# Performance work log

Measured on AMD Instinct MI355X. Metric: run time of the kernel, lower is better.

The kernel has to match this reference:

```python
import jax, jax.numpy as jnp
import numpy as np

BH, W, C, NHEAD = 512, 256, 128, 4
HEAD_DIM = C // NHEAD
EPS = 1e-5


def _xavier(key, shape):
    fan_out, fan_in = shape
    lim = np.sqrt(6.0 / (fan_in + fan_out)).astype(np.float32)
    return jax.random.uniform(key, shape, jnp.float32, -lim, lim)


def setup_inputs() -> dict:
    key = jax.random.key(0)
    ks = jax.random.split(key, 4)
    return {
        "feat_left": jax.random.normal(ks[0], (BH, W, C), jnp.float32),
        "feat_right": jax.random.normal(ks[1], (BH, W, C), jnp.float32),
        "l_proj_weight": _xavier(ks[2], (2 * C, C)),
        "r_proj_weight": _xavier(ks[3], (2 * C, C)),
        "l_proj_bias": jnp.zeros((2 * C,), jnp.float32),
        "r_proj_bias": jnp.zeros((2 * C,), jnp.float32),
        "l_out_weight": _xavier(jax.random.fold_in(key, 10), (C, C)),
        "l_out_bias": jnp.zeros((C,), jnp.float32),
        "r_out_weight": _xavier(jax.random.fold_in(key, 11), (C, C)),
        "r_out_bias": jnp.zeros((C,), jnp.float32),
        "norm_weight": jnp.ones((C,), jnp.float32),
        "norm_bias": jnp.zeros((C,), jnp.float32),
    }


def _layernorm(x, w, b):
    mu = jnp.mean(x, axis=-1, keepdims=True)
    var = jnp.mean(jnp.square(x - mu), axis=-1, keepdims=True)
    return (x - mu) * jax.lax.rsqrt(var + EPS) * w + b


def reference(feat_left, feat_right, l_proj_weight, r_proj_weight,
              l_proj_bias, r_proj_bias, l_out_weight, l_out_bias,
              r_out_weight, r_out_bias, norm_weight, norm_bias):
    bh, w, c = feat_left.shape
    e, hd = NHEAD, HEAD_DIM

    l_n = _layernorm(feat_left, norm_weight, norm_bias)
    r_n = _layernorm(feat_right, norm_weight, norm_bias)

    l_kv = l_n @ l_proj_weight.T + l_proj_bias
    r_kv = r_n @ r_proj_weight.T + r_proj_bias
    l_k, l_v = jnp.split(l_kv, 2, axis=-1)
    r_k, r_v = jnp.split(r_kv, 2, axis=-1)

    l_k = l_k.reshape(bh, w, e, hd)
    r_k = r_k.reshape(bh, w, e, hd)
    l_v = l_v.reshape(bh, w, e, hd)
    r_v = r_v.reshape(bh, w, e, hd)

    # shared score matrix [bh, heads, w_left, w_right]
    attn = jnp.einsum('nwec,nvec->newv', l_k, r_k) * 0.1

    # left attends over right positions (softmax over last axis)
    sm_l = jax.nn.softmax(attn, axis=-1)
    out_l = jnp.einsum('newv,nvec->nwec', sm_l, r_v).reshape(bh, w, c)

    # right attends over left positions (softmax over w axis of same scores)
    sm_r = jax.nn.softmax(attn, axis=2)
    out_r = jnp.einsum('newv,nwec->nvec', sm_r, l_v).reshape(bh, w, c)

    out_l = out_l @ l_out_weight.T + l_out_bias
    out_r = out_r @ r_out_weight.T + r_out_bias

    return feat_left + out_l, feat_right + out_r
```

## Files before the change

### kernel.cpp

```cpp
#include <hip/hip_runtime.h>
#include <hip/hip_bf16.h>

#define BH   512
#define NW   256
#define CC   128
#define TOK  (BH * NW)

typedef __attribute__((ext_vector_type(8))) short short8;
typedef __attribute__((ext_vector_type(4))) float f32x4;
typedef __attribute__((ext_vector_type(4))) int   i32x4;
typedef __attribute__((ext_vector_type(4))) unsigned short us4;
typedef __attribute__((ext_vector_type(2))) unsigned int u32x2;
typedef unsigned short ushort_t;

static __device__ __forceinline__ f32x4 mfma16(short8 a, short8 b, f32x4 c) {
    return __builtin_amdgcn_mfma_f32_16x16x32_bf16(a, b, c, 0, 0, 0);
}

static __device__ __forceinline__ unsigned int pk2(float a, float b) {
    __hip_bfloat162 h = __float22bfloat162_rn(make_float2(a, b));
    return *reinterpret_cast<unsigned int*>(&h);
}
static __device__ __forceinline__ ushort_t f2bf(float f) {
    unsigned int u = __float_as_uint(f);
    u = (u + 0x7fffu + ((u >> 16) & 1u)) >> 16;
    return (ushort_t)u;
}
#if __has_builtin(__builtin_amdgcn_exp2f)
static __device__ __forceinline__ float exp2_fast(float x) { return __builtin_amdgcn_exp2f(x); }
#else
static __device__ __forceinline__ float exp2_fast(float x) { return exp2f(x); }
#endif

__global__ __launch_bounds__(256)
void k_prep(const float* __restrict__ WpL, const float* __restrict__ WpR,
            const float* __restrict__ bpL, const float* __restrict__ bpR,
            const float* __restrict__ nw,  const float* __restrict__ nb,
            ushort_t* __restrict__ Wb, float* __restrict__ bias2)
{
    const int gid = blockIdx.x * 256 + threadIdx.x;
    const int row = gid >> 2;
    const int q   = gid & 3;
    const int side = row >> 8;
    const int o    = row & 255;
    const float* Wp = side ? WpR : WpL;
    const float* bp = side ? bpR : bpL;
    const float* wr = Wp + (size_t)o * 128 + q * 32;

    float acc = 0.f;
#pragma unroll
    for (int g = 0; g < 4; ++g) {
        const int c = q * 32 + g * 8;
        float4 wa = *(const float4*)(wr + g * 8);
        float4 wb = *(const float4*)(wr + g * 8 + 4);
        float4 ga = *(const float4*)(nw + c);
        float4 gb = *(const float4*)(nw + c + 4);
        float4 ba = *(const float4*)(nb + c);
        float4 bb = *(const float4*)(nb + c + 4);
        acc += wa.x*ba.x + wa.y*ba.y + wa.z*ba.z + wa.w*ba.w
             + wb.x*bb.x + wb.y*bb.y + wb.z*bb.z + wb.w*bb.w;
        u32x2 o0, o1;
        o0[0] = pk2(wa.x*ga.x, wa.y*ga.y);
        o0[1] = pk2(wa.z*ga.z, wa.w*ga.w);
        o1[0] = pk2(wb.x*gb.x, wb.y*gb.y);
        o1[1] = pk2(wb.z*gb.z, wb.w*gb.w);
        *(u32x2*)(Wb + (size_t)row * 128 + c)     = o0;
        *(u32x2*)(Wb + (size_t)row * 128 + c + 4) = o1;
    }
    acc += __shfl_xor(acc, 1);
    acc += __shfl_xor(acc, 2);
    if (q == 0) bias2[row] = bp[o] + acc;
}

__global__ __launch_bounds__(512)
void k_ln_proj(const float* __restrict__ featL, const float* __restrict__ featR,
               const ushort_t* __restrict__ Wb, const float* __restrict__ bias2,
               ushort_t* __restrict__ kvL,      ushort_t* __restrict__ kvR)
{
    const int side = blockIdx.y;
    const float* feat = side ? featR : featL;
    const ushort_t* W = Wb + side * 32768;
    const float* b2   = bias2 + side * 256;
    ushort_t*    kv   = side ? kvR : kvL;

    const int m0  = blockIdx.x * 64;
    const int tid = threadIdx.x;
    const int wid = tid >> 6, lane = tid & 63, l16 = lane & 15, lh = lane >> 4;
    const int wn  = wid * 32;

    __shared__ ushort_t Asm[64][136];

    const int row = tid >> 3, q = tid & 7;
    const float* fr = feat + (size_t)(m0 + row) * CC + q * 16;
    float x[16];
#pragma unroll
    for (int i = 0; i < 4; ++i) {
        float4 v = *(const float4*)(fr + i * 4);
        x[i*4+0]=v.x; x[i*4+1]=v.y; x[i*4+2]=v.z; x[i*4+3]=v.w;
    }

    short8 Bf[8];
#pragma unroll
    for (int kk = 0; kk < 4; ++kk)
#pragma unroll
        for (int tn = 0; tn < 2; ++tn)
            Bf[kk*2 + tn] = *(const short8*)(W + (size_t)(wn + tn*16 + l16) * CC + kk*32 + lh*8);
    float4 bias[2];
#pragma unroll
    for (int tn = 0; tn < 2; ++tn)
        bias[tn] = *(const float4*)(b2 + wn + tn*16 + lh*4);

    {
        float s = 0.f, s2 = 0.f;
#pragma unroll
        for (int i = 0; i < 16; ++i) { s += x[i]; s2 += x[i]*x[i]; }
#pragma unroll
        for (int m = 1; m < 8; m <<= 1) { s += __shfl_xor(s, m); s2 += __shfl_xor(s2, m); }
        float mu   = s * (1.f / 128.f);
        float var  = s2 * (1.f / 128.f) - mu * mu;
        float rstd = rsqrtf(var + 1e-5f);
        float a = rstd, bsh = -mu * rstd;
#pragma unroll
        for (int g = 0; g < 2; ++g) {
            i32x4 o;
#pragma unroll
            for (int k = 0; k < 4; ++k)
                o[k] = (int)pk2(x[g*8 + 2*k] * a + bsh, x[g*8 + 2*k + 1] * a + bsh);
            *(i32x4*)&Asm[row][q * 16 + g * 8] = o;
        }
    }
    __syncthreads();

    f32x4 acc[4][2];
#pragma unroll
    for (int mt = 0; mt < 4; ++mt)
#pragma unroll
        for (int tn = 0; tn < 2; ++tn)
            acc[mt][tn] = (f32x4){0.f, 0.f, 0.f, 0.f};

#pragma unroll
    for (int kk = 0; kk < 4; ++kk) {
        short8 a[4];
#pragma unroll
        for (int mt = 0; mt < 4; ++mt)
            a[mt] = *(const short8*)&Asm[mt*16 + l16][kk*32 + lh*8];
#pragma unroll
        for (int tn = 0; tn < 2; ++tn)
#pragma unroll
            for (int mt = 0; mt < 4; ++mt)
                acc[mt][tn] = mfma16(Bf[kk*2 + tn], a[mt], acc[mt][tn]);
    }

    const float kscale = (side == 0 && wn < 128) ? 0.14426950408889634f : 1.0f;
#pragma unroll
    for (int mt = 0; mt < 4; ++mt) {
        const int token = m0 + mt*16 + l16;
#pragma unroll
        for (int tn = 0; tn < 2; ++tn) {
            const int f0 = wn + tn*16 + lh*4;
            float v0 = (acc[mt][tn][0] + bias[tn].x) * kscale;
            float v1 = (acc[mt][tn][1] + bias[tn].y) * kscale;
            float v2 = (acc[mt][tn][2] + bias[tn].z) * kscale;
            float v3 = (acc[mt][tn][3] + bias[tn].w) * kscale;
            u32x2 wv;
            wv[0] = pk2(v0, v1);
            wv[1] = pk2(v2, v3);
            *(u32x2*)(kv + (size_t)token * 256 + f0) = wv;
        }
    }
}

template<int BF16OUT>
__global__ __launch_bounds__(512, 4)
void k_attn(const ushort_t* __restrict__ kvL, const ushort_t* __restrict__ kvR,
            float* __restrict__ outFBase, ushort_t* __restrict__ outBBase)
{
    const int bx   = blockIdx.x;
    const int work = (bx & 7) * 512 + (bx >> 3);
    const int n    = work >> 3;
    const int e    = (work >> 1) & 3;
    const int dir  = work & 1;
    const ushort_t* kvA = dir ? kvR : kvL;
    const ushort_t* kvB = dir ? kvL : kvR;

    const int tid = threadIdx.x;
    const int wid = tid >> 6, lane = tid & 63, l16 = lane & 15, lh = lane >> 4;
    const int W0 = wid * 32;
    const int kcls = (l16 >> 1) & 3;

    __shared__ ushort_t kB[256][32];
    __shared__ ushort_t vT[32][280];
    __shared__ ushort_t pL[8][32][32];

    {
        const ushort_t* src = kvB + (size_t)n * 256 * 256 + e * 32;
#pragma unroll
        for (int p = 0; p < 2; ++p) {
            int u = tid + p * 512;
            int r = u >> 2, slot = u & 3;
            *(i32x4*)&kB[r][(slot ^ ((r >> 1) & 3)) << 3] =
                *(const i32x4*)(src + (size_t)r * 256 + slot * 8);
        }
    }
    {
        const ushort_t* src = kvB + (size_t)n * 256 * 256 + 128 + e * 32;
#pragma unroll
        for (int u4 = 0; u4 < 4; ++u4) {
            int unit = tid + u4 * 512;
            int cp = unit & 15, vp = unit >> 4;
            unsigned int w0 = *(const unsigned int*)(src + (size_t)(vp*2    ) * 256 + cp*2);
            unsigned int w1 = *(const unsigned int*)(src + (size_t)(vp*2 + 1) * 256 + cp*2);
            *(unsigned int*)&vT[cp*2    ][vp*2] = (w0 & 0xffffu) | (w1 << 16);
            *(unsigned int*)&vT[cp*2 + 1][vp*2] = (w0 >> 16) | (w1 & 0xffff0000u);
        }
    }
    short8 aK[2];
#pragma unroll
    for (int tr = 0; tr < 2; ++tr)
        aK[tr] = *(const short8*)(kvA + (size_t)(n*256 + W0 + tr*16 + l16) * 256 + e*32 + lh*8);

    short8 ones;
#pragma unroll
    for (int i = 0; i < 8; ++i) ones[i] = (short)0x3F80;

    __syncthreads();

    f32x4 oacc[2][2];
#pragma unroll
    for (int tr = 0; tr < 2; ++tr)
#pragma unroll
        for (int ct = 0; ct < 2; ++ct)
            oacc[tr][ct] = (f32x4){0.f, 0.f, 0.f, 0.f};
    f32x4 lacc[2] = {(f32x4){0.f,0.f,0.f,0.f}, (f32x4){0.f,0.f,0.f,0.f}};

#pragma unroll 2
    for (int nc = 0; nc < 8; ++nc) {
        const int vc0 = nc * 32;

        short8 bk0 = *(const short8*)&kB[vc0      + l16][(lh ^ kcls) << 3];
        short8 bk1 = *(const short8*)&kB[vc0 + 16 + l16][(lh ^ kcls) << 3];
        f32x4 s[2][2];
#pragma unroll
        for (int tr = 0; tr < 2; ++tr) {
            s[tr][0] = mfma16(bk0, aK[tr], (f32x4){0.f,0.f,0.f,0.f});
            s[tr][1] = mfma16(bk1, aK[tr], (f32x4){0.f,0.f,0.f,0.f});
        }

#pragma unroll
        for (int tr = 0; tr < 2; ++tr) {
            const int prow = tr*16 + l16;
#pragma unroll
            for (int tc = 0; tc < 2; ++tc) {
                float p0 = exp2_fast(s[tr][tc][0]);
                float p1 = exp2_fast(s[tr][tc][1]);
                float p2 = exp2_fast(s[tr][tc][2]);
                float p3 = exp2_fast(s[tr][tc][3]);
                u32x2 w;
                w[0] = pk2(p0, p1);
                w[1] = pk2(p2, p3);
                const int sL   = 2*tc + (lh >> 1);
                const int pcol = ((sL ^ kcls) << 3) + ((lh & 1) << 2);
                *(u32x2*)&pL[wid][prow][pcol] = w;
            }
        }

        short8 aP[2], bV[2];
#pragma unroll
        for (int tr = 0; tr < 2; ++tr)
            aP[tr] = *(const short8*)&pL[wid][tr*16 + l16][(lh ^ kcls) << 3];
#pragma unroll
        for (int ct = 0; ct < 2; ++ct)
            bV[ct] = *(const short8*)&vT[ct*16 + l16][vc0 + lh*8];
#pragma unroll
        for (int tr = 0; tr < 2; ++tr) {
#pragma unroll
            for (int ct = 0; ct < 2; ++ct)
                oacc[tr][ct] = mfma16(bV[ct], aP[tr], oacc[tr][ct]);
            lacc[tr] = mfma16(ones, aP[tr], lacc[tr]);
        }
    }

#pragma unroll
    for (int tr = 0; tr < 2; ++tr) {
        float rinv = 1.f / lacc[tr][0];
        const int token = n * 256 + W0 + tr*16 + l16;
        if (BF16OUT) {
            ushort_t* outB = outBBase + (size_t)dir * TOK * CC;
#pragma unroll
            for (int ct = 0; ct < 2; ++ct) {
                us4 o;
#pragma unroll
                for (int j = 0; j < 4; ++j)
                    o[j] = f2bf(oacc[tr][ct][j] * rinv);
                *(us4*)(outB + (size_t)token * CC + e*32 + ct*16 + lh*4) = o;
            }
        } else {
            float* outF = outFBase + (size_t)dir * TOK * CC;
#pragma unroll
            for (int ct = 0; ct < 2; ++ct) {
                float4 o;
                o.x = oacc[tr][ct][0] * rinv;
                o.y = oacc[tr][ct][1] * rinv;
                o.z = oacc[tr][ct][2] * rinv;
                o.w = oacc[tr][ct][3] * rinv;
                *(float4*)(outF + (size_t)token * CC + e*32 + ct*16 + lh*4) = o;
            }
        }
    }
}

template<int BF16IN>
__global__ __launch_bounds__(512, 4)
void k_outproj(float* __restrict__ outBase, const ushort_t* __restrict__ aoutBase,
               const float* __restrict__ featL, const float* __restrict__ featR,
               const float* __restrict__ WoL,   const float* __restrict__ WoR,
               const float* __restrict__ boL,   const float* __restrict__ boR)
{
    const int side = blockIdx.y;
    float* io = outBase + (size_t)side * TOK * CC;
    const float* feat = side ? featR : featL;
    const float* Wo   = side ? WoR   : WoL;
    const float* bo   = side ? boR   : boL;

    const int m0 = blockIdx.x * 64;
    const int tid = threadIdx.x;
    const int wid = tid >> 6, lane = tid & 63, l16 = lane & 15, lh = lane >> 4;
    const int wm = (wid >> 2) * 32;
    const int wn = (wid & 3) * 32;

    __shared__ ushort_t Asm[64][136];
    __shared__ ushort_t Wsm[128][136];

    float4 bias4[2];
#pragma unroll
    for (int nt = 0; nt < 2; ++nt)
        bias4[nt] = *(const float4*)(bo + wn + nt*16 + lh*4);

#pragma unroll
    for (int i = 0; i < 8; ++i) {
        int u = tid + i * 512;
        int r = u >> 5, c4 = (u & 31) * 4;
        float4 w4 = *(const float4*)(Wo + (size_t)r * CC + c4);
        Wsm[r][c4+0] = f2bf(w4.x); Wsm[r][c4+1] = f2bf(w4.y);
        Wsm[r][c4+2] = f2bf(w4.z); Wsm[r][c4+3] = f2bf(w4.w);
    }
    if (BF16IN) {
        const ushort_t* src = aoutBase + (size_t)side * TOK * CC;
#pragma unroll
        for (int i = 0; i < 2; ++i) {
            int u = tid + i * 512;
            int r = u >> 4, c0 = (u & 15) * 8;
            *(i32x4*)&Asm[r][c0] = *(const i32x4*)(src + (size_t)(m0 + r) * CC + c0);
        }
    } else {
#pragma unroll
        for (int i = 0; i < 4; ++i) {
            int u = tid + i * 512;
            int r = u >> 5, c4 = (u & 31) * 4;
            float4 a4 = *(const float4*)(io + (size_t)(m0 + r) * CC + c4);
            Asm[r][c4+0] = f2bf(a4.x); Asm[r][c4+1] = f2bf(a4.y);
            Asm[r][c4+2] = f2bf(a4.z); Asm[r][c4+3] = f2bf(a4.w);
        }
    }
    __syncthreads();

    f32x4 acc[2][2];
#pragma unroll
    for (int tr = 0; tr < 2; ++tr)
#pragma unroll
        for (int nt = 0; nt < 2; ++nt)
            acc[tr][nt] = (f32x4){0.f, 0.f, 0.f, 0.f};

#pragma unroll
    for (int kk = 0; kk < 4; ++kk) {
        short8 a[2], b[2];
#pragma unroll
        for (int tr = 0; tr < 2; ++tr)
            a[tr] = *(const short8*)&Asm[wm + tr*16 + l16][kk*32 + lh*8];
#pragma unroll
        for (int nt = 0; nt < 2; ++nt)
            b[nt] = *(const short8*)&Wsm[wn + nt*16 + l16][kk*32 + lh*8];
#pragma unroll
        for (int tr = 0; tr < 2; ++tr)
#pragma unroll
            for (int nt = 0; nt < 2; ++nt)
                acc[tr][nt] = mfma16(b[nt], a[tr], acc[tr][nt]);
    }

#pragma unroll
    for (int tr = 0; tr < 2; ++tr) {
        const int token = m0 + wm + tr*16 + l16;
#pragma unroll
        for (int nt = 0; nt < 2; ++nt) {
            const int f0 = wn + nt*16 + lh*4;
            float4 ff = *(const float4*)(feat + (size_t)token * CC + f0);
            float4 o;
            o.x = acc[tr][nt][0] + bias4[nt].x + ff.x;
            o.y = acc[tr][nt][1] + bias4[nt].y + ff.y;
            o.z = acc[tr][nt][2] + bias4[nt].z + ff.z;
            o.w = acc[tr][nt][3] + bias4[nt].w + ff.w;
            *(float4*)(io + (size_t)token * CC + f0) = o;
        }
    }
}

extern "C" void kernel_launch(void* const* d_in, const int* in_sizes, int n_in,
                              void* d_out, int out_size, void* d_ws, size_t ws_size,
                              hipStream_t stream)
{
    const float* featL = (const float*)d_in[0];
    const float* featR = (const float*)d_in[1];
    const float* WpL   = (const float*)d_in[2];
    const float* WpR   = (const float*)d_in[3];
    const float* bpL   = (const float*)d_in[4];
    const float* bpR   = (const float*)d_in[5];
    const float* WoL   = (const float*)d_in[6];
    const float* boL   = (const float*)d_in[7];
    const float* WoR   = (const float*)d_in[8];
    const float* boR   = (const float*)d_in[9];
    const float* nw    = (const float*)d_in[10];
    const float* nb    = (const float*)d_in[11];

    float* out = (float*)d_out;
    ushort_t* kvL = (ushort_t*)d_ws;
    ushort_t* kvR = kvL + (size_t)TOK * 256;
    ushort_t* aout = kvR + (size_t)TOK * 256;
    ushort_t* Wb  = (ushort_t*)d_out;
    float* bias2  = (float*)d_out + 32768;

    const size_t need_bf16 = (size_t)TOK * 256 * 2 * 2 + (size_t)TOK * CC * 2 * 2;
    const bool bf16path = ws_size >= need_bf16;

    k_prep<<<dim3(8), 256, 0, stream>>>(WpL, WpR, bpL, bpR, nw, nb, Wb, bias2);
    k_ln_proj<<<dim3(2048, 2), 512, 0, stream>>>(featL, featR, Wb, bias2, kvL, kvR);
    if (bf16path) {
        k_attn<1><<<dim3(4096), 512, 0, stream>>>(kvL, kvR, out, aout);
        k_outproj<1><<<dim3(TOK / 64, 2), 512, 0, stream>>>(out, aout, featL, featR,
                                                            WoL, WoR, boL, boR);
    } else {
        k_attn<0><<<dim3(4096), 512, 0, stream>>>(kvL, kvR, out, aout);
        k_outproj<0><<<dim3(TOK / 64, 2), 512, 0, stream>>>(out, aout, featL, featR,
                                                            WoL, WoR, boL, boR);
    }
}
```

Measured before the change: 219.2 us.

## Pre-convert out-proj weights to bf16 and coalesce kv stores via LDS staging

The prep kernel now also converts both output-projection weights to bf16 once, so the out-projection kernel loads its weight fragments straight into registers rather than converting fp32 weights into shared memory in every block. The ln_proj epilogue stages its results in a shared-memory tile and writes them back as full contiguous rows, replacing the scattered 8-byte stores. The weight scratch moves into the workspace on the bf16 path. These changes add shared-memory use and an extra barrier in ln_proj and more register pressure in the out-projection.

```diff
diff --git a/kernel.cpp b/kernel.cpp
--- a/kernel.cpp
+++ b/kernel.cpp
@@ -35,41 +35,63 @@
 __global__ __launch_bounds__(256)
 void k_prep(const float* __restrict__ WpL, const float* __restrict__ WpR,
             const float* __restrict__ bpL, const float* __restrict__ bpR,
+            const float* __restrict__ WoL, const float* __restrict__ WoR,
             const float* __restrict__ nw,  const float* __restrict__ nb,
-            ushort_t* __restrict__ Wb, float* __restrict__ bias2)
+            ushort_t* __restrict__ Wb, float* __restrict__ bias2,
+            ushort_t* __restrict__ WoB)
 {
-    const int gid = blockIdx.x * 256 + threadIdx.x;
-    const int row = gid >> 2;
-    const int q   = gid & 3;
-    const int side = row >> 8;
-    const int o    = row & 255;
-    const float* Wp = side ? WpR : WpL;
-    const float* bp = side ? bpR : bpL;
-    const float* wr = Wp + (size_t)o * 128 + q * 32;
-
-    float acc = 0.f;
-#pragma unroll
-    for (int g = 0; g < 4; ++g) {
-        const int c = q * 32 + g * 8;
-        float4 wa = *(const float4*)(wr + g * 8);
-        float4 wb = *(const float4*)(wr + g * 8 + 4);
-        float4 ga = *(const float4*)(nw + c);
-        float4 gb = *(const float4*)(nw + c + 4);
-        float4 ba = *(const float4*)(nb + c);
-        float4 bb = *(const float4*)(nb + c + 4);
-        acc += wa.x*ba.x + wa.y*ba.y + wa.z*ba.z + wa.w*ba.w
-             + wb.x*bb.x + wb.y*bb.y + wb.z*bb.z + wb.w*bb.w;
-        u32x2 o0, o1;
-        o0[0] = pk2(wa.x*ga.x, wa.y*ga.y);
-        o0[1] = pk2(wa.z*ga.z, wa.w*ga.w);
-        o1[0] = pk2(wb.x*gb.x, wb.y*gb.y);
-        o1[1] = pk2(wb.z*gb.z, wb.w*gb.w);
-        *(u32x2*)(Wb + (size_t)row * 128 + c)     = o0;
-        *(u32x2*)(Wb + (size_t)row * 128 + c + 4) = o1;
-    }
-    acc += __shfl_xor(acc, 1);
-    acc += __shfl_xor(acc, 2);
-    if (q == 0) bias2[row] = bp[o] + acc;
+    if (blockIdx.x < 8) {
+        const int gid = blockIdx.x * 256 + threadIdx.x;
+        const int row = gid >> 2;
+        const int q   = gid & 3;
+        const int side = row >> 8;
+        const int o    = row & 255;
+        const float* Wp = side ? WpR : WpL;
+        const float* bp = side ? bpR : bpL;
+        const float* wr = Wp + (size_t)o * 128 + q * 32;
+
+        float acc = 0.f;
+#pragma unroll
+        for (int g = 0; g < 4; ++g) {
+            const int c = q * 32 + g * 8;
+            float4 wa = *(const float4*)(wr + g * 8);
+            float4 wb = *(const float4*)(wr + g * 8 + 4);
+            float4 ga = *(const float4*)(nw + c);
+            float4 gb = *(const float4*)(nw + c + 4);
+            float4 ba = *(const float4*)(nb + c);
+            float4 bb = *(const float4*)(nb + c + 4);
+            acc += wa.x*ba.x + wa.y*ba.y + wa.z*ba.z + wa.w*ba.w
+                 + wb.x*bb.x + wb.y*bb.y + wb.z*bb.z + wb.w*bb.w;
+            u32x2 o0, o1;
+            o0[0] = pk2(wa.x*ga.x, wa.y*ga.y);
+            o0[1] = pk2(wa.z*ga.z, wa.w*ga.w);
+            o1[0] = pk2(wb.x*gb.x, wb.y*gb.y);
+            o1[1] = pk2(wb.z*gb.z, wb.w*gb.w);
+            *(u32x2*)(Wb + (size_t)row * 128 + c)     = o0;
+            *(u32x2*)(Wb + (size_t)row * 128 + c + 4) = o1;
+        }
+        acc += __shfl_xor(acc, 1);
+        acc += __shfl_xor(acc, 2);
+        if (q == 0) bias2[row] = bp[o] + acc;
+    } else {
+        const int idx  = (blockIdx.x - 8) * 256 + threadIdx.x;
+        const int row2 = idx >> 2;
+        const int q    = idx & 3;
+        const int side = row2 >> 7;
+        const int o    = row2 & 127;
+        const float* Wo = side ? WoR : WoL;
+        const float* wr = Wo + (size_t)o * 128 + q * 32;
+#pragma unroll
+        for (int g = 0; g < 4; ++g) {
+            float4 wa = *(const float4*)(wr + g * 8);
+            float4 wb = *(const float4*)(wr + g * 8 + 4);
+            u32x2 o0, o1;
+            o0[0] = pk2(wa.x, wa.y); o0[1] = pk2(wa.z, wa.w);
+            o1[0] = pk2(wb.x, wb.y); o1[1] = pk2(wb.z, wb.w);
+            *(u32x2*)(WoB + (size_t)row2 * 128 + q * 32 + g * 8)     = o0;
+            *(u32x2*)(WoB + (size_t)row2 * 128 + q * 32 + g * 8 + 4) = o1;
+        }
+    }
 }
 
 __global__ __launch_bounds__(512)
@@ -89,6 +111,7 @@
     const int wn  = wid * 32;
 
     __shared__ ushort_t Asm[64][136];
+    __shared__ ushort_t kvS[64][260];
 
     const int row = tid >> 3, q = tid & 7;
     const float* fr = feat + (size_t)(m0 + row) * CC + q * 16;
@@ -153,11 +176,11 @@
 
     const float kscale = (side == 0 && wn < 128) ? 0.14426950408889634f : 1.0f;
 #pragma unroll
-    for (int mt = 0; mt < 4; ++mt) {
-        const int token = m0 + mt*16 + l16;
+    for (int mt = 0; mt < 4; ++mt)
 #pragma unroll
         for (int tn = 0; tn < 2; ++tn) {
-            const int f0 = wn + tn*16 + lh*4;
+            const int r    = mt*16 + l16;
+            const int slot = (wn >> 2) + tn*4 + lh;
             float v0 = (acc[mt][tn][0] + bias[tn].x) * kscale;
             float v1 = (acc[mt][tn][1] + bias[tn].y) * kscale;
             float v2 = (acc[mt][tn][2] + bias[tn].z) * kscale;
@@ -165,8 +188,16 @@
             u32x2 wv;
             wv[0] = pk2(v0, v1);
             wv[1] = pk2(v2, v3);
-            *(u32x2*)(kv + (size_t)token * 256 + f0) = wv;
-        }
+            *(u32x2*)&kvS[r][slot * 4] = wv;
+        }
+    __syncthreads();
+
+#pragma unroll
+    for (int it = 0; it < 8; ++it) {
+        int u = it * 512 + tid;
+        int r = u >> 6, sl = u & 63;
+        u32x2 wv = *(const u32x2*)&kvS[r][sl * 4];
+        *(u32x2*)(kv + (size_t)(m0 + r) * 256 + sl * 4) = wv;
     }
 }
 
@@ -309,12 +340,90 @@
     }
 }
 
-template<int BF16IN>
+__global__ __launch_bounds__(512)
+void k_outproj_fast(float* __restrict__ outBase, const ushort_t* __restrict__ aoutBase,
+                    const float* __restrict__ featL, const float* __restrict__ featR,
+                    const ushort_t* __restrict__ WoB,
+                    const float* __restrict__ boL, const float* __restrict__ boR)
+{
+    const int side = blockIdx.y;
+    float* io = outBase + (size_t)side * TOK * CC;
+    const float* feat = side ? featR : featL;
+    const ushort_t* Wo = WoB + side * 16384;
+    const float* bo   = side ? boR : boL;
+
+    const int m0 = blockIdx.x * 64;
+    const int tid = threadIdx.x;
+    const int wid = tid >> 6, lane = tid & 63, l16 = lane & 15, lh = lane >> 4;
+    const int wm = (wid >> 2) * 32;
+    const int wn = (wid & 3) * 32;
+
+    __shared__ ushort_t Asm[64][136];
+
+    short8 Bf[8];
+#pragma unroll
+    for (int kk = 0; kk < 4; ++kk)
+#pragma unroll
+        for (int tn = 0; tn < 2; ++tn)
+            Bf[kk*2 + tn] = *(const short8*)(Wo + (size_t)(wn + tn*16 + l16) * CC + kk*32 + lh*8);
+    float4 bias4[2];
+#pragma unroll
+    for (int nt = 0; nt < 2; ++nt)
+        bias4[nt] = *(const float4*)(bo + wn + nt*16 + lh*4);
+
+    {
+        const ushort_t* src = aoutBase + (size_t)side * TOK * CC;
+#pragma unroll
+        for (int i = 0; i < 2; ++i) {
+            int u = tid + i * 512;
+            int r = u >> 4, c0 = (u & 15) * 8;
+            *(i32x4*)&Asm[r][c0] = *(const i32x4*)(src + (size_t)(m0 + r) * CC + c0);
+        }
+    }
+    __syncthreads();
+
+    f32x4 acc[2][2];
+#pragma unroll
+    for (int tr = 0; tr < 2; ++tr)
+#pragma unroll
+        for (int nt = 0; nt < 2; ++nt)
+            acc[tr][nt] = (f32x4){0.f, 0.f, 0.f, 0.f};
+
+#pragma unroll
+    for (int kk = 0; kk < 4; ++kk) {
+        short8 a[2];
+#pragma unroll
+        for (int tr = 0; tr < 2; ++tr)
+            a[tr] = *(const short8*)&Asm[wm + tr*16 + l16][kk*32 + lh*8];
+#pragma unroll
+        for (int tr = 0; tr < 2; ++tr)
+#pragma unroll
+            for (int nt = 0; nt < 2; ++nt)
+                acc[tr][nt] = mfma16(Bf[kk*2 + nt], a[tr], acc[tr][nt]);
+    }
+
+#pragma unroll
+    for (int tr = 0; tr < 2; ++tr) {
+        const int token = m0 + wm + tr*16 + l16;
+#pragma unroll
+        for (int nt = 0; nt < 2; ++nt) {
+            const int f0 = wn + nt*16 + lh*4;
+            float4 ff = *(const float4*)(feat + (size_t)token * CC + f0);
+            float4 o;
+            o.x = acc[tr][nt][0] + bias4[nt].x + ff.x;
+            o.y = acc[tr][nt][1] + bias4[nt].y + ff.y;
+            o.z = acc[tr][nt][2] + bias4[nt].z + ff.z;
+            o.w = acc[tr][nt][3] + bias4[nt].w + ff.w;
+            *(float4*)(io + (size_t)token * CC + f0) = o;
+        }
+    }
+}
+
 __global__ __launch_bounds__(512, 4)
-void k_outproj(float* __restrict__ outBase, const ushort_t* __restrict__ aoutBase,
-               const float* __restrict__ featL, const float* __restrict__ featR,
-               const float* __restrict__ WoL,   const float* __restrict__ WoR,
-               const float* __restrict__ boL,   const float* __restrict__ boR)
+void k_outproj_slow(float* __restrict__ outBase,
+                    const float* __restrict__ featL, const float* __restrict__ featR,
+                    const float* __restrict__ WoL,   const float* __restrict__ WoR,
+                    const float* __restrict__ boL,   const float* __restrict__ boR)
 {
     const int side = blockIdx.y;
     float* io = outBase + (size_t)side * TOK * CC;
@@ -341,26 +450,16 @@
         int u = tid + i * 512;
         int r = u >> 5, c4 = (u & 31) * 4;
         float4 w4 = *(const float4*)(Wo + (size_t)r * CC + c4);
-        Wsm[r][c4+0] = f2bf(w4.x); Wsm[r][c4+1] = f2bf(w4.y);
-        Wsm[r][c4+2] = f2bf(w4.z); Wsm[r][c4+3] = f2bf(w4.w);
-    }
-    if (BF16IN) {
-        const ushort_t* src = aoutBase + (size_t)side * TOK * CC;
-#pragma unroll
-        for (int i = 0; i < 2; ++i) {
-            int u = tid + i * 512;
-            int r = u >> 4, c0 = (u & 15) * 8;
-            *(i32x4*)&Asm[r][c0] = *(const i32x4*)(src + (size_t)(m0 + r) * CC + c0);
-        }
-    } else {
-#pragma unroll
-        for (int i = 0; i < 4; ++i) {
-            int u = tid + i * 512;
-            int r = u >> 5, c4 = (u & 31) * 4;
-            float4 a4 = *(const float4*)(io + (size_t)(m0 + r) * CC + c4);
-            Asm[r][c4+0] = f2bf(a4.x); Asm[r][c4+1] = f2bf(a4.y);
-            Asm[r][c4+2] = f2bf(a4.z); Asm[r][c4+3] = f2bf(a4.w);
-        }
+        u32x2 wv; wv[0] = pk2(w4.x, w4.y); wv[1] = pk2(w4.z, w4.w);
+        *(u32x2*)&Wsm[r][c4] = wv;
+    }
+#pragma unroll
+    for (int i = 0; i < 4; ++i) {
+        int u = tid + i * 512;
+        int r = u >> 5, c4 = (u & 31) * 4;
+        float4 a4 = *(const float4*)(io + (size_t)(m0 + r) * CC + c4);
+        u32x2 av; av[0] = pk2(a4.x, a4.y); av[1] = pk2(a4.z, a4.w);
+        *(u32x2*)&Asm[r][c4] = av;
     }
     __syncthreads();
 
@@ -425,21 +524,33 @@
     ushort_t* kvL = (ushort_t*)d_ws;
     ushort_t* kvR = kvL + (size_t)TOK * 256;
     ushort_t* aout = kvR + (size_t)TOK * 256;
-    ushort_t* Wb  = (ushort_t*)d_out;
-    float* bias2  = (float*)d_out + 32768;
-
-    const size_t need_bf16 = (size_t)TOK * 256 * 2 * 2 + (size_t)TOK * CC * 2 * 2;
-    const bool bf16path = ws_size >= need_bf16;
-
-    k_prep<<<dim3(8), 256, 0, stream>>>(WpL, WpR, bpL, bpR, nw, nb, Wb, bias2);
-    k_ln_proj<<<dim3(2048, 2), 512, 0, stream>>>(featL, featR, Wb, bias2, kvL, kvR);
+
+    const size_t kv_us   = (size_t)TOK * 256 * 2;
+    const size_t aout_us = (size_t)TOK * CC * 2;
+    const size_t wscr_us = 65536 + 1024 + 32768;
+    const bool bf16path = ws_size >= (kv_us + aout_us + wscr_us) * 2;
+
     if (bf16path) {
+        ushort_t* Wb  = aout + aout_us;
+        float* bias2  = (float*)(Wb + 65536);
+        ushort_t* WoB = (ushort_t*)(bias2 + 512);
+
+        k_prep<<<dim3(12), 256, 0, stream>>>(WpL, WpR, bpL, bpR, WoL, WoR,
+                                             nw, nb, Wb, bias2, WoB);
+        k_ln_proj<<<dim3(2048, 2), 512, 0, stream>>>(featL, featR, Wb, bias2, kvL, kvR);
         k_attn<1><<<dim3(4096), 512, 0, stream>>>(kvL, kvR, out, aout);
-        k_outproj<1><<<dim3(TOK / 64, 2), 512, 0, stream>>>(out, aout, featL, featR,
-                                                            WoL, WoR, boL, boR);
+        k_outproj_fast<<<dim3(TOK / 64, 2), 512, 0, stream>>>(out, aout, featL, featR,
+                                                              WoB, boL, boR);
     } else {
+        ushort_t* Wb  = (ushort_t*)d_out;
+        float* bias2  = (float*)d_out + 32768;
+        ushort_t* WoB = (ushort_t*)d_out + 66560;
+
+        k_prep<<<dim3(12), 256, 0, stream>>>(WpL, WpR, bpL, bpR, WoL, WoR,
+                                             nw, nb, Wb, bias2, WoB);
+        k_ln_proj<<<dim3(2048, 2), 512, 0, stream>>>(featL, featR, Wb, bias2, kvL, kvR);
         k_attn<0><<<dim3(4096), 512, 0, stream>>>(kvL, kvR, out, aout);
-        k_outproj<0><<<dim3(TOK / 64, 2), 512, 0, stream>>>(out, aout, featL, featR,
-                                                            WoL, WoR, boL, boR);
-    }
-}
+        k_outproj_slow<<<dim3(TOK / 64, 2), 512, 0, stream>>>(out, featL, featR,
+                                                              WoL, WoR, boL, boR);
+    }
+}
```

After: 207.5 us. 1.06x faster.
